# Optimization experiments

Hardware: AMD Instinct MI355X
Metric: run time of the kernel (lower is better)

## Reference

```python
import jax, jax.numpy as jnp
import numpy as np


def conv(x, w, b=None, stride=1, pad=0):
    out = jax.lax.conv_general_dilated(
        x, w, (stride, stride), ((pad, pad), (pad, pad)),
        dimension_numbers=('NCHW', 'OIHW', 'NCHW'))
    if b is not None:
        out = out + b[None, :, None, None]
    return out


def conv_transpose_4s2p1(x, w, b):
    # PyTorch ConvTranspose2d(k=4, stride=2, pad=1) == lhs-dilated conv,
    # pad = k - 1 - p = 2 each side; output spatial = 2 * input.
    out = jax.lax.conv_general_dilated(
        x, w, (1, 1), ((2, 2), (2, 2)), lhs_dilation=(2, 2),
        dimension_numbers=('NCHW', 'OIHW', 'NCHW'))
    return out + b[None, :, None, None]


def res_stack(h, blocks):
    # block: x + Conv1x1(ReLU(Conv3x3(ReLU(x)))); final ReLU after stack
    for wa, wb in blocks:
        r = conv(jax.nn.relu(h), wa, None, 1, 1)
        r = conv(jax.nn.relu(r), wb, None, 1, 0)
        h = h + r
    return jax.nn.relu(h)


def setup_inputs() -> dict:
    key = jax.random.key(0)
    ks = iter(jax.random.split(key, 32))
    H = 128  # num_hiddens
    RH = 32  # num_residual_hiddens
    K, D = 512, 64  # num_embeddings, embedding_dim
    B = 32

    def w(shape, fan_in):
        s = 1.0 / np.sqrt(fan_in)
        return jax.random.uniform(next(ks), shape, jnp.float32, -s, s)

    inp = {}
    inp['x'] = jax.random.normal(next(ks), (B, 3, 128, 128), jnp.float32)
    # encoder
    inp['e_w1'] = w((H // 2, 3, 4, 4), 3 * 16); inp['e_b1'] = w((H // 2,), 3 * 16)
    inp['e_w2'] = w((H, H // 2, 4, 4), H // 2 * 16); inp['e_b2'] = w((H,), H // 2 * 16)
    inp['e_w3'] = w((H, H, 3, 3), H * 9); inp['e_b3'] = w((H,), H * 9)
    inp['e_r1a'] = w((RH, H, 3, 3), H * 9); inp['e_r1b'] = w((H, RH, 1, 1), RH)
    inp['e_r2a'] = w((RH, H, 3, 3), H * 9); inp['e_r2b'] = w((H, RH, 1, 1), RH)
    # pre-VQ 1x1 conv
    inp['pre_w'] = w((D, H, 1, 1), H); inp['pre_b'] = w((D,), H)
    # codebook: uniform(-1/K, 1/K)
    inp['codebook'] = jax.random.uniform(next(ks), (K, D), jnp.float32, -1.0 / K, 1.0 / K)
    # decoder
    inp['d_w1'] = w((H, D, 3, 3), D * 9); inp['d_b1'] = w((H,), D * 9)
    inp['d_r1a'] = w((RH, H, 3, 3), H * 9); inp['d_r1b'] = w((H, RH, 1, 1), RH)
    inp['d_r2a'] = w((RH, H, 3, 3), H * 9); inp['d_r2b'] = w((H, RH, 1, 1), RH)
    inp['dt_w1'] = w((H // 2, H, 4, 4), H * 16); inp['dt_b1'] = w((H // 2,), H * 16)
    inp['dt_w2'] = w((3, H // 2, 4, 4), H // 2 * 16); inp['dt_b2'] = w((3,), H // 2 * 16)
    return inp


def reference(x, e_w1, e_b1, e_w2, e_b2, e_w3, e_b3, e_r1a, e_r1b, e_r2a, e_r2b,
              pre_w, pre_b, codebook, d_w1, d_b1, d_r1a, d_r1b, d_r2a, d_r2b,
              dt_w1, dt_b1, dt_w2, dt_b2):
    beta = 0.25  # commitment cost
    K = codebook.shape[0]
    # ----- encoder -----
    h = jax.nn.relu(conv(x, e_w1, e_b1, 2, 1))
    h = jax.nn.relu(conv(h, e_w2, e_b2, 2, 1))
    h = conv(h, e_w3, e_b3, 1, 1)
    h = res_stack(h, [(e_r1a, e_r1b), (e_r2a, e_r2b)])
    z = conv(h, pre_w, pre_b, 1, 0)  # [B, D, h, w]
    # ----- vector quantizer -----
    zl = jnp.transpose(z, (0, 2, 3, 1))  # [B, h, w, D]
    flat = zl.reshape(-1, zl.shape[-1])  # [N, D]
    d2 = (jnp.sum(flat * flat, axis=1, keepdims=True)
          + jnp.sum(codebook * codebook, axis=1)
          - 2.0 * flat @ codebook.T)  # [N, K]
    idx = jnp.argmin(d2, axis=1)  # [N]
    enc = jax.nn.one_hot(idx, K, dtype=flat.dtype)  # [N, K]
    q = codebook[idx].reshape(zl.shape)  # == enc @ codebook
    q_latent = jnp.mean((jax.lax.stop_gradient(q) - zl) ** 2)
    e_latent = jnp.mean((q - jax.lax.stop_gradient(zl)) ** 2)
    loss = q_latent + beta * e_latent
    q_st = zl + jax.lax.stop_gradient(q - zl)  # straight-through
    avg_probs = jnp.mean(enc, axis=0)
    perplexity = jnp.exp(-jnp.sum(avg_probs * jnp.log(avg_probs + 1e-10)))
    qc = jnp.transpose(q_st, (0, 3, 1, 2))  # [B, D, h, w]
    # ----- decoder -----
    g = conv(qc, d_w1, d_b1, 1, 1)
    g = res_stack(g, [(d_r1a, d_r1b), (d_r2a, d_r2b)])
    g = jax.nn.relu(conv_transpose_4s2p1(g, dt_w1, dt_b1))
    x_recon = conv_transpose_4s2p1(g, dt_w2, dt_b2)
    return (loss, x_recon, perplexity)
```

## Files before the change

### kernel.cpp

```cpp
#include <hip/hip_runtime.h>


typedef short short8 __attribute__((ext_vector_type(8)));
typedef float f32x4 __attribute__((ext_vector_type(4)));
typedef unsigned short us;

__device__ __forceinline__ us f2bf(float f) {
    unsigned u = __builtin_bit_cast(unsigned, f);
    u += 0x7fffu + ((u >> 16) & 1u);
    return (us)(u >> 16);
}
__device__ __forceinline__ float bf2f(us b) {
    unsigned u = ((unsigned)b) << 16;
    return __builtin_bit_cast(float, u);
}
__device__ __forceinline__ void gload_lds16(const void* g, void* l) {
    __builtin_amdgcn_global_load_lds(
        (const __attribute__((address_space(1))) void*)g,
        (__attribute__((address_space(3))) void*)l, 16, 0, 0);
}

template<bool SPLIT, int MI, int NI, int ASTR, int APLANE, int BPLANE>
__device__ __forceinline__ void mfma_step32(
    const us* lsA, const us* lsB, f32x4* acc, int wm0, int wn0, int l)
{
    short8 ah[MI], bh[NI];
    #pragma unroll
    for (int mi = 0; mi < MI; ++mi)
        ah[mi] = *(const short8*)&lsA[(wm0 + mi*16 + (l&15))*ASTR + (l>>4)*8];
    #pragma unroll
    for (int ni = 0; ni < NI; ++ni)
        bh[ni] = *(const short8*)&lsB[(wn0 + ni*16 + (l&15))*32 + (l>>4)*8];
    if (SPLIT) {
        short8 al[MI], bl[NI];
        #pragma unroll
        for (int mi = 0; mi < MI; ++mi)
            al[mi] = *(const short8*)&lsA[APLANE + (wm0 + mi*16 + (l&15))*ASTR + (l>>4)*8];
        #pragma unroll
        for (int ni = 0; ni < NI; ++ni)
            bl[ni] = *(const short8*)&lsB[BPLANE + (wn0 + ni*16 + (l&15))*32 + (l>>4)*8];
        #pragma unroll
        for (int mi = 0; mi < MI; ++mi)
            #pragma unroll
            for (int ni = 0; ni < NI; ++ni) {
                acc[mi*NI+ni] = __builtin_amdgcn_mfma_f32_16x16x32_bf16(ah[mi], bh[ni], acc[mi*NI+ni], 0, 0, 0);
                acc[mi*NI+ni] = __builtin_amdgcn_mfma_f32_16x16x32_bf16(ah[mi], bl[ni], acc[mi*NI+ni], 0, 0, 0);
                acc[mi*NI+ni] = __builtin_amdgcn_mfma_f32_16x16x32_bf16(al[mi], bh[ni], acc[mi*NI+ni], 0, 0, 0);
            }
    } else {
        #pragma unroll
        for (int mi = 0; mi < MI; ++mi)
            #pragma unroll
            for (int ni = 0; ni < NI; ++ni)
                acc[mi*NI+ni] = __builtin_amdgcn_mfma_f32_16x16x32_bf16(ah[mi], bh[ni], acc[mi*NI+ni], 0, 0, 0);
    }
}

template<int CIN, int KH, int KW, int S, bool FP32IN, bool SPLIT,
         int BN, int WM_, int WN_, bool BIAS, int RESID, bool RELU, bool DUAL,
         int OMODE, bool BK64>
__global__ __launch_bounds__(256, 4) void conv_gemm(
    const us* __restrict__ inH, const us* __restrict__ inL,
    const float* __restrict__ inF,
    const us* __restrict__ Wp, unsigned long long wloff,
    const float* __restrict__ bias,
    us* __restrict__ oH, us* __restrict__ oL,
    us* __restrict__ o2H, us* __restrict__ o2L,
    float* __restrict__ oF,
    const us* __restrict__ rH, const us* __restrict__ rL,
    const us* __restrict__ zpage,
    int Hin, int Win, int Wout, int HWout, int Cout, int pady, int padx,
    int py, int px, int nbn)
{
    constexpr int BM = 64;
    constexpr int K = CIN * KH * KW;
    constexpr int KP = ((K + 31) / 32) * 32;
    constexpr int TAPS = KH * KW;
    constexpr int ASTR = FP32IN ? 40 : 32;
    constexpr int ASHORT = FP32IN ? BM*40 : (BK64 ? BM*64 : BM*32);
    constexpr int BSHORT = (BK64 && !FP32IN) ? BN*64 : BN*32;
    constexpr int MI = BM / WM_ / 16, NI = BN / WN_ / 16;
    constexpr bool PIX1 = (KH == 1 && KW == 1 && S == 1);
    __shared__ __align__(16) us lsA[(SPLIT ? 2 : 1) * ASHORT];
    __shared__ __align__(16) us lsB[(SPLIT ? 2 : 1) * BSHORT];

    int t = threadIdx.x, l = t & 63, w = t >> 6;
    int bid = blockIdx.x;
    int nt = bid % nbn;
    int tm = (bid / nbn) * BM;
    int ncol0 = nt * BN;
    const us* Wt = Wp + (size_t)ncol0 * KP;
    int wm0 = (w / WN_) * (BM / WM_);
    int wn0 = (w % WN_) * (BN / WN_);
    f32x4 acc[MI * NI] = {};
    const int e0 = t * 8;

    if (FP32IN) {
        int m_l = t & 63, kseg = t >> 6;
        int ms = tm + m_l;
        int bsv = ms / HWout; int remv = ms - bsv * HWout;
        int oys = remv / Wout, oxs = remv - (remv / Wout) * Wout;
        int iy0 = oys * S - pady, ix0 = oxs * S - padx;
        const float* ibase = inF + (size_t)bsv * CIN * Hin * Win;
        for (int k0 = 0; k0 < KP; k0 += 32) {
            if (e0 < BN * 32) {
                size_t gb = (size_t)(e0 >> 5) * KP + k0 + (e0 & 31);
                gload_lds16(Wt + gb, &lsB[e0]);
                if (SPLIT) gload_lds16(Wt + wloff + gb, &lsB[BSHORT + e0]);
            }
            short8 hi, lo;
            #pragma unroll
            for (int j = 0; j < 8; ++j) {
                int k = k0 + kseg * 8 + j;
                float v = 0.f;
                if (k < K) {
                    int tap = k / CIN, c = k - tap * CIN;
                    int ky = tap / KW, kx = tap - (tap / KW) * KW;
                    int iy = iy0 + ky, ix = ix0 + kx;
                    if ((unsigned)iy < (unsigned)Hin && (unsigned)ix < (unsigned)Win)
                        v = ibase[((size_t)c * Hin + iy) * Win + ix];
                }
                us hb = f2bf(v);
                hi[j] = (short)hb;
                if (SPLIT) lo[j] = (short)f2bf(v - bf2f(hb));
            }
            *(short8*)&lsA[m_l * ASTR + kseg * 8] = hi;
            if (SPLIT) *(short8*)&lsA[ASHORT + m_l * ASTR + kseg * 8] = lo;
            __syncthreads();
            mfma_step32<SPLIT, MI, NI, ASTR, ASHORT, BSHORT>(lsA, lsB, acc, wm0, wn0, l);
            __syncthreads();
        }
    } else if (!BK64) {
        int mrow = t >> 2;
        int lane8 = (t & 3) * 8;
        int m = tm + mrow;
        int bsv = m / HWout; int remv = m - bsv * HWout;
        int oys = remv / Wout, oxs = remv - oys * Wout;
        int iy0 = oys * S - pady, ix0 = oxs * S - padx;
        #pragma unroll
        for (int tap = 0; tap < TAPS; ++tap) {
            int ky = tap / KW, kx = tap - (tap / KW) * KW;
            int iy = iy0 + ky, ix = ix0 + kx;
            bool ok = PIX1 || ((unsigned)iy < (unsigned)Hin && (unsigned)ix < (unsigned)Win);
            size_t pix = ((size_t)bsv * Hin + iy) * Win + ix;
            const us* phi = ok ? inH + pix * CIN + lane8 : zpage + lane8;
            const us* plo = zpage;
            if (SPLIT) plo = ok ? inL + pix * CIN + lane8 : zpage + lane8;
            #pragma unroll
            for (int cc = 0; cc < CIN; cc += 32) {
                const int k0 = tap * CIN + cc;
                if (e0 < BN * 32) {
                    size_t gb = (size_t)(e0 >> 5) * KP + k0 + (e0 & 31);
                    gload_lds16(Wt + gb, &lsB[e0]);
                    if (SPLIT) gload_lds16(Wt + wloff + gb, &lsB[BSHORT + e0]);
                }
                gload_lds16(phi + cc, &lsA[t * 8]);
                if (SPLIT) gload_lds16(plo + cc, &lsA[ASHORT + t * 8]);
                __syncthreads();
                mfma_step32<SPLIT, MI, NI, ASTR, ASHORT, BSHORT>(lsA, lsB, acc, wm0, wn0, l);
                __syncthreads();
            }
        }
    } else {
        int r0 = t >> 3;
        int lc8 = (((t & 7) ^ (t >> 3)) & 7) * 8;
        int m0v = tm + r0, m1v = tm + r0 + 32;
        int bs0 = m0v / HWout, rm0 = m0v - bs0 * HWout;
        int oy0 = rm0 / Wout, ox0 = rm0 - oy0 * Wout;
        int bs1 = m1v / HWout, rm1 = m1v - bs1 * HWout;
        int oy1 = rm1 / Wout, ox1 = rm1 - oy1 * Wout;
        int iy00 = oy0 * S - pady, ix00 = ox0 * S - padx;
        int iy10 = oy1 * S - pady, ix10 = ox1 * S - padx;
        #pragma unroll
        for (int tap = 0; tap < TAPS; ++tap) {
            int ky = tap / KW, kx = tap - (tap / KW) * KW;
            int iyA = iy00 + ky, ixA = ix00 + kx;
            int iyB = iy10 + ky, ixB = ix10 + kx;
            bool okA = PIX1 || ((unsigned)iyA < (unsigned)Hin && (unsigned)ixA < (unsigned)Win);
            bool okB = PIX1 || ((unsigned)iyB < (unsigned)Hin && (unsigned)ixB < (unsigned)Win);
            size_t pxA = ((size_t)bs0 * Hin + iyA) * Win + ixA;
            size_t pxB = ((size_t)bs1 * Hin + iyB) * Win + ixB;
            const us* pA = okA ? inH + pxA * CIN + lc8 : zpage + lc8;
            const us* pB = okB ? inH + pxB * CIN + lc8 : zpage + lc8;
            const us* qA = zpage + lc8;
            const us* qB = zpage + lc8;
            if (SPLIT) {
                qA = okA ? inL + pxA * CIN + lc8 : zpage + lc8;
                qB = okB ? inL + pxB * CIN + lc8 : zpage + lc8;
            }
            #pragma unroll
            for (int cc = 0; cc < CIN; cc += 64) {
                const int k0 = tap * CIN + cc;
                #pragma unroll
                for (int q = 0; q < (BN + 31) / 32; ++q) {
                    if (BN >= 32 || t < BN * 8) {
                        size_t gb = (size_t)(q * 32 + (t >> 3)) * KP + k0 + (t & 7) * 8;
                        gload_lds16(Wt + gb, &lsB[q * 2048 + t * 8]);
                        if (SPLIT) gload_lds16(Wt + wloff + gb, &lsB[BSHORT + q * 2048 + t * 8]);
                    }
                }
                gload_lds16(pA + cc, &lsA[t * 8]);
                gload_lds16(pB + cc, &lsA[2048 + t * 8]);
                if (SPLIT) {
                    gload_lds16(qA + cc, &lsA[ASHORT + t * 8]);
                    gload_lds16(qB + cc, &lsA[ASHORT + 2048 + t * 8]);
                }
                __syncthreads();
                #pragma unroll
                for (int kk = 0; kk < 2; ++kk) {
                    short8 ah[MI], bh[NI];
                    #pragma unroll
                    for (int mi = 0; mi < MI; ++mi) {
                        int row = wm0 + mi * 16 + (l & 15);
                        int pc = (kk * 4 + (l >> 4)) ^ (row & 7);
                        ah[mi] = *(const short8*)&lsA[row * 64 + pc * 8];
                    }
                    #pragma unroll
                    for (int ni = 0; ni < NI; ++ni) {
                        int row = wn0 + ni * 16 + (l & 15);
                        int pc = (kk * 4 + (l >> 4)) ^ (row & 7);
                        bh[ni] = *(const short8*)&lsB[row * 64 + pc * 8];
                    }
                    if (SPLIT) {
                        short8 al[MI], bl[NI];
                        #pragma unroll
                        for (int mi = 0; mi < MI; ++mi) {
                            int row = wm0 + mi * 16 + (l & 15);
                            int pc = (kk * 4 + (l >> 4)) ^ (row & 7);
                            al[mi] = *(const short8*)&lsA[ASHORT + row * 64 + pc * 8];
                        }
                        #pragma unroll
                        for (int ni = 0; ni < NI; ++ni) {
                            int row = wn0 + ni * 16 + (l & 15);
                            int pc = (kk * 4 + (l >> 4)) ^ (row & 7);
                            bl[ni] = *(const short8*)&lsB[BSHORT + row * 64 + pc * 8];
                        }
                        #pragma unroll
                        for (int mi = 0; mi < MI; ++mi)
                            #pragma unroll
                            for (int ni = 0; ni < NI; ++ni) {
                                acc[mi*NI+ni] = __builtin_amdgcn_mfma_f32_16x16x32_bf16(ah[mi], bh[ni], acc[mi*NI+ni], 0, 0, 0);
                                acc[mi*NI+ni] = __builtin_amdgcn_mfma_f32_16x16x32_bf16(ah[mi], bl[ni], acc[mi*NI+ni], 0, 0, 0);
                                acc[mi*NI+ni] = __builtin_amdgcn_mfma_f32_16x16x32_bf16(al[mi], bh[ni], acc[mi*NI+ni], 0, 0, 0);
                            }
                    } else {
                        #pragma unroll
                        for (int mi = 0; mi < MI; ++mi)
                            #pragma unroll
                            for (int ni = 0; ni < NI; ++ni)
                                acc[mi*NI+ni] = __builtin_amdgcn_mfma_f32_16x16x32_bf16(ah[mi], bh[ni], acc[mi*NI+ni], 0, 0, 0);
                    }
                }
                __syncthreads();
            }
        }
    }

    #pragma unroll
    for (int mi = 0; mi < MI; ++mi) {
        #pragma unroll
        for (int ni = 0; ni < NI; ++ni) {
            int n = ncol0 + wn0 + ni * 16 + (l & 15);
            if (n >= Cout) continue;
            float bv = BIAS ? bias[n] : 0.f;
            #pragma unroll
            for (int j = 0; j < 4; ++j) {
                int m = tm + wm0 + mi * 16 + (l >> 4) * 4 + j;
                float v = acc[mi * NI + ni][j] + bv;
                if (RESID == 1) { size_t ri = (size_t)m * Cout + n; v += bf2f(rH[ri]) + bf2f(rL[ri]); }
                if (RESID == 2) { v += bf2f(rH[(size_t)m * Cout + n]); }
                float vr = RELU ? fmaxf(v, 0.f) : v;
                if (DUAL) {
                    size_t oi = (size_t)m * Cout + n;
                    us hb = f2bf(v);
                    o2H[oi] = hb;
                    if (SPLIT) o2L[oi] = f2bf(v - bf2f(hb));
                }
                if (OMODE == 0) {
                    size_t oi = (size_t)m * Cout + n;
                    us hb = f2bf(vr);
                    oH[oi] = hb;
                    if (SPLIT) oL[oi] = f2bf(vr - bf2f(hb));
                } else if (OMODE == 1) {
                    int b2 = m / HWout, rem = m - b2 * HWout;
                    oF[(size_t)(b2 * Cout + n) * HWout + rem] = vr;
                } else if (OMODE == 2) {
                    int b2 = m / HWout, rem = m - b2 * HWout;
                    int y = rem / Wout, x2 = rem - y * Wout;
                    oF[(size_t)(b2 * Cout + n) * (4 * HWout)
                       + (size_t)(2 * y + py) * (2 * Wout) + (2 * x2 + px)] = vr;
                } else {
                    int b2 = m / HWout, rem = m - b2 * HWout;
                    int y = rem / Wout, x2 = rem - y * Wout;
                    int Hg2 = 2 * (HWout / Wout);
                    size_t oi = (((size_t)b2 * Hg2 + (2 * y + py)) * (size_t)(2 * Wout)
                                 + (2 * x2 + px)) * Cout + n;
                    oH[oi] = f2bf(vr);
                }
            }
        }
    }
}

struct PackDesc {
    const float* src; unsigned long long dstoff;
    int Npad, N, CIN, KH, KW, K, Kpad, mode, py, px, split, swz;
};
struct PackArgs { PackDesc d[21]; };

__global__ __launch_bounds__(256) void wpack_all(PackArgs pa, us* __restrict__ wp)
{
    PackDesc d = pa.d[blockIdx.y];
    int gid = blockIdx.x * 256 + threadIdx.x;
    int tot = d.Npad * d.Kpad;
    if (gid >= tot) return;
    int n = gid / d.Kpad;
    int k = gid - n * d.Kpad;
    int klog = k;
    if (d.swz) {
        int kb = k >> 6, pc = (k >> 3) & 7, j = k & 7;
        klog = (kb << 6) + (((pc ^ (n & 7)) & 7) << 3) + j;
    }
    float v = 0.0f;
    if (n < d.N && klog < d.K) {
        int tap = klog / d.CIN, c = klog - tap * d.CIN;
        int ky, kx;
        if (d.mode == 0) { ky = tap / d.KW; kx = tap - (tap / d.KW) * d.KW; }
        else { int ty = tap >> 1, tx = tap & 1; ky = d.py + 2 * ty; kx = d.px + 2 * tx; }
        v = d.src[((size_t)(n * d.CIN + c) * d.KH + ky) * d.KW + kx];
    }
    us hb = f2bf(v);
    wp[d.dstoff + gid] = hb;
    if (d.split) wp[d.dstoff + tot + gid] = f2bf(v - bf2f(hb));
}

__global__ __launch_bounds__(256) void vq_sq(
    const float* __restrict__ cb, float* __restrict__ ccsq)
{
    int k = blockIdx.x * 256 + threadIdx.x;
    const float* c = cb + (size_t)k * 64;
    float a0 = 0.f, a1 = 0.f;
    #pragma unroll
    for (int d = 0; d < 64; d += 2) {
        a0 = fmaf(c[d], c[d], a0);
        a1 = fmaf(c[d + 1], c[d + 1], a1);
    }
    ccsq[k] = a0 + a1;
}

__global__ __launch_bounds__(256) void vq_scan(
    const float* __restrict__ z, const float* __restrict__ cb,
    const float* __restrict__ ccsq,
    float* __restrict__ pdist, int* __restrict__ pidx)
{
    const int HW = 1024;
    int n = blockIdx.x * 256 + threadIdx.x;
    int chunk = blockIdx.y;
    int base = chunk * 64;
    int b = n >> 10;
    int p = n & 1023;
    const float* zp = z + (size_t)b * 64 * HW + p;
    float zv[64];
    #pragma unroll
    for (int d = 0; d < 64; ++d) zv[d] = zp[(size_t)d * HW];

    float best = 3.402823e38f;
    int bi = base;
    for (int kk = 0; kk < 64; kk += 2) {
        const float* c0 = cb + (size_t)(base + kk) * 64;
        float a0 = 0.f, a1 = 0.f, b0 = 0.f, b1 = 0.f;
        #pragma unroll
        for (int d = 0; d < 64; d += 2) {
            a0 = fmaf(zv[d],     c0[d],          a0);
            a1 = fmaf(zv[d + 1], c0[d + 1],      a1);
            b0 = fmaf(zv[d],     c0[64 + d],     b0);
            b1 = fmaf(zv[d + 1], c0[64 + d + 1], b1);
        }
        float s0 = ccsq[base + kk]     - 2.0f * (a0 + a1);
        float s1 = ccsq[base + kk + 1] - 2.0f * (b0 + b1);
        if (s0 < best) { best = s0; bi = base + kk; }
        if (s1 < best) { best = s1; bi = base + kk + 1; }
    }
    pdist[(size_t)chunk * 32768 + n] = best;
    pidx [(size_t)chunk * 32768 + n] = bi;
}

__global__ __launch_bounds__(256) void vq_reduce(
    const float* __restrict__ z, const float* __restrict__ cb,
    const float* __restrict__ pdist, const int* __restrict__ pidx,
    us* __restrict__ qb, int* __restrict__ idxbuf, float* __restrict__ sse)
{
    const int HW = 1024;
    int nl = threadIdx.x & 31;
    int dg = threadIdx.x >> 5;
    int n = blockIdx.x * 32 + nl;
    float best = pdist[n];
    int bi = pidx[n];
    #pragma unroll
    for (int ch = 1; ch < 8; ++ch) {
        float dv = pdist[(size_t)ch * 32768 + n];
        int iv = pidx[(size_t)ch * 32768 + n];
        if (dv < best) { best = dv; bi = iv; }
    }
    if (dg == 0) idxbuf[n] = bi;
    int b = n >> 10;
    int p = n & 1023;
    const float* zp = z + (size_t)b * 64 * HW + p;
    const float* c = cb + (size_t)bi * 64;
    float s = 0.f;
    short8 qv;
    #pragma unroll
    for (int j = 0; j < 8; ++j) {
        int d = dg * 8 + j;
        float q = c[d];
        qv[j] = (short)f2bf(q);
        float df = q - zp[(size_t)d * HW];
        s = fmaf(df, df, s);
    }
    *(short8*)&qb[(size_t)n * 64 + dg * 8] = qv;
    #pragma unroll
    for (int off = 32; off > 0; off >>= 1) s += __shfl_down(s, off, 64);
    __shared__ float red[4];
    if ((threadIdx.x & 63) == 0) red[threadIdx.x >> 6] = s;
    __syncthreads();
    if (threadIdx.x == 0) atomicAdd(sse, red[0] + red[1] + red[2] + red[3]);
}

__global__ __launch_bounds__(1024) void vq_hist(
    const int* __restrict__ idxbuf, float* __restrict__ hist)
{
    __shared__ int lh[512];
    int t = threadIdx.x;
    if (t < 512) lh[t] = 0;
    __syncthreads();
    #pragma unroll
    for (int j = 0; j < 32; ++j)
        atomicAdd(&lh[idxbuf[j * 1024 + t]], 1);
    __syncthreads();
    if (t < 512) hist[t] = (float)lh[t];
}

__global__ __launch_bounds__(512) void vq_finalize(
    const float* __restrict__ hist, const float* __restrict__ sse,
    float* __restrict__ out_loss, float* __restrict__ out_ppl)
{
    __shared__ float red[512];
    int t = threadIdx.x;
    float p = hist[t] * (1.0f / 32768.0f);
    red[t] = p * logf(p + 1e-10f);
    __syncthreads();
    for (int s = 256; s > 0; s >>= 1) {
        if (t < s) red[t] += red[t + s];
        __syncthreads();
    }
    if (t == 0) {
        *out_ppl = expf(-red[0]);
        *out_loss = 1.25f * (*sse) * (1.0f / 2097152.0f);
    }
}

extern "C" void kernel_launch(void* const* d_in, const int* in_sizes, int n_in,
                              void* d_out, int out_size, void* d_ws, size_t ws_size,
                              hipStream_t stream)
{
    const float* x        = (const float*)d_in[0];
    const float* e_w1     = (const float*)d_in[1];
    const float* e_b1     = (const float*)d_in[2];
    const float* e_w2     = (const float*)d_in[3];
    const float* e_b2     = (const float*)d_in[4];
    const float* e_w3     = (const float*)d_in[5];
    const float* e_b3     = (const float*)d_in[6];
    const float* e_r1a    = (const float*)d_in[7];
    const float* e_r1b    = (const float*)d_in[8];
    const float* e_r2a    = (const float*)d_in[9];
    const float* e_r2b    = (const float*)d_in[10];
    const float* pre_w    = (const float*)d_in[11];
    const float* pre_b    = (const float*)d_in[12];
    const float* codebook = (const float*)d_in[13];
    const float* d_w1     = (const float*)d_in[14];
    const float* d_b1     = (const float*)d_in[15];
    const float* d_r1a    = (const float*)d_in[16];
    const float* d_r1b    = (const float*)d_in[17];
    const float* d_r2a    = (const float*)d_in[18];
    const float* d_r2b    = (const float*)d_in[19];
    const float* dt_w1    = (const float*)d_in[20];
    const float* dt_b1    = (const float*)d_in[21];
    const float* dt_w2    = (const float*)d_in[22];
    const float* dt_b2    = (const float*)d_in[23];
    float* out = (float*)d_out;

    const size_t MB = 1024 * 1024;
    char* base = (char*)d_ws;
    char* A0 = base;
    char* B0 = base + 32 * MB;
    char* C0 = base + 48 * MB;
    char* D0 = base + 64 * MB;
    float* st = (float*)(base + 68 * MB);
    us* wp = (us*)(base + 68 * MB + 4096);

    us* h1H = (us*)A0;              us* h1L = (us*)(A0 + 16 * MB);
    us* hBH = (us*)B0;              us* hBL = (us*)(B0 + 8 * MB);
    us* CeH = (us*)A0;              us* CeL = (us*)(A0 + 8 * MB);
    us* CrH = (us*)C0;              us* CrL = (us*)(C0 + 8 * MB);
    us* DsH = (us*)D0;              us* DsL = (us*)(D0 + 2 * MB);
    us* T2rH = (us*)A0;             us* T2rL = (us*)(A0 + 8 * MB);
    us* T2eH = (us*)B0;             us* T2eL = (us*)(B0 + 8 * MB);
    us* T3H = (us*)C0;              us* T3L = (us*)(C0 + 8 * MB);
    float* E = (float*)B0;
    us* qb = (us*)(B0 + 8 * MB);
    float* pdist = (float*)A0;
    int* pidx = (int*)(A0 + 1 * MB);
    int* idxbuf = (int*)(A0 + 2 * MB);
    float* ccsq = (float*)(A0 + 2 * MB + 128 * 1024);
    us* GeH = (us*)A0;              us* GrH = (us*)(A0 + 8 * MB);
    us* dDs = (us*)D0;
    us* dT2e = (us*)B0;             us* dT2r = (us*)(B0 + 8 * MB);
    us* dT3 = (us*)C0;
    us* gbuf = (us*)A0;
    const us* zpage = (const us*)(st + 576);

    PackArgs pa;
    int np = 0; unsigned long long wpo = 0;
    auto addpack = [&](const float* src, int N, int Npad, int CIN, int KH, int KW,
                       int K, int Kpad, int mode, int py, int px, int split,
                       int swz) -> unsigned long long {
        pa.d[np].src = src; pa.d[np].dstoff = wpo;
        pa.d[np].Npad = Npad; pa.d[np].N = N; pa.d[np].CIN = CIN;
        pa.d[np].KH = KH; pa.d[np].KW = KW; pa.d[np].K = K; pa.d[np].Kpad = Kpad;
        pa.d[np].mode = mode; pa.d[np].py = py; pa.d[np].px = px;
        pa.d[np].split = split; pa.d[np].swz = swz;
        ++np; unsigned long long off = wpo; wpo += (unsigned long long)Npad * Kpad * (split ? 2 : 1);
        return off;
    };
    unsigned long long P_E1  = addpack(e_w1, 64, 64, 3, 4, 4, 48, 64, 0, 0, 0, 1, 0);
    unsigned long long P_E2  = addpack(e_w2, 128, 128, 64, 4, 4, 1024, 1024, 0, 0, 0, 1, 1);
    unsigned long long P_E3  = addpack(e_w3, 128, 128, 128, 3, 3, 1152, 1152, 0, 0, 0, 1, 1);
    unsigned long long P_R1A = addpack(e_r1a, 32, 32, 128, 3, 3, 1152, 1152, 0, 0, 0, 1, 1);
    unsigned long long P_R1B = addpack(e_r1b, 128, 128, 32, 1, 1, 32, 32, 0, 0, 0, 1, 0);
    unsigned long long P_R2A = addpack(e_r2a, 32, 32, 128, 3, 3, 1152, 1152, 0, 0, 0, 1, 1);
    unsigned long long P_R2B = addpack(e_r2b, 128, 128, 32, 1, 1, 32, 32, 0, 0, 0, 1, 0);
    unsigned long long P_PRE = addpack(pre_w, 64, 64, 128, 1, 1, 128, 128, 0, 0, 0, 1, 1);
    unsigned long long P_D1  = addpack(d_w1, 128, 128, 64, 3, 3, 576, 576, 0, 0, 0, 0, 1);
    unsigned long long P_DR1A = addpack(d_r1a, 32, 32, 128, 3, 3, 1152, 1152, 0, 0, 0, 0, 1);
    unsigned long long P_DR1B = addpack(d_r1b, 128, 128, 32, 1, 1, 32, 32, 0, 0, 0, 0, 0);
    unsigned long long P_DR2A = addpack(d_r2a, 32, 32, 128, 3, 3, 1152, 1152, 0, 0, 0, 0, 1);
    unsigned long long P_DR2B = addpack(d_r2b, 128, 128, 32, 1, 1, 32, 32, 0, 0, 0, 0, 0);
    unsigned long long P_DT1[4], P_DT2[4];
    for (int p = 0; p < 4; ++p)
        P_DT1[p] = addpack(dt_w1, 64, 64, 128, 4, 4, 512, 512, 1, p >> 1, p & 1, 0, 1);
    for (int p = 0; p < 4; ++p)
        P_DT2[p] = addpack(dt_w2, 3, 16, 64, 4, 4, 256, 256, 1, p >> 1, p & 1, 0, 1);

    hipMemsetAsync(st, 0, 4096, stream);
    wpack_all<<<dim3(576, 21), 256, 0, stream>>>(pa, wp);

    conv_gemm<3,4,4,2, true,true, 64,2,2, true,0,true,false,0, false><<<dim3(2048),256,0,stream>>>(
        nullptr, nullptr, x, wp + P_E1, 64ull*64, e_b1,
        h1H, h1L, nullptr, nullptr, nullptr, nullptr, nullptr, zpage,
        128,128, 64, 4096, 64, 1,1, 0,0, 1);
    conv_gemm<64,4,4,2, false,true, 64,2,2, true,0,true,false,0, true><<<dim3(1024),256,0,stream>>>(
        h1H, h1L, nullptr, wp + P_E2, 128ull*1024, e_b2,
        hBH, hBL, nullptr, nullptr, nullptr, nullptr, nullptr, zpage,
        64,64, 32, 1024, 128, 1,1, 0,0, 2);
    conv_gemm<128,3,3,1, false,true, 64,2,2, true,0,true,true,0, true><<<dim3(1024),256,0,stream>>>(
        hBH, hBL, nullptr, wp + P_E3, 128ull*1152, e_b3,
        CeH, CeL, CrH, CrL, nullptr, nullptr, nullptr, zpage,
        32,32, 32, 1024, 128, 1,1, 0,0, 2);
    conv_gemm<128,3,3,1, false,true, 32,4,1, false,0,true,false,0, true><<<dim3(512),256,0,stream>>>(
        CeH, CeL, nullptr, wp + P_R1A, 32ull*1152, nullptr,
        DsH, DsL, nullptr, nullptr, nullptr, nullptr, nullptr, zpage,
        32,32, 32, 1024, 32, 1,1, 0,0, 1);
    conv_gemm<32,1,1,1, false,true, 64,2,2, false,1,true,true,0, false><<<dim3(1024),256,0,stream>>>(
        DsH, DsL, nullptr, wp + P_R1B, 128ull*32, nullptr,
        T2eH, T2eL, T2rH, T2rL, nullptr, CrH, CrL, zpage,
        32,32, 32, 1024, 128, 0,0, 0,0, 2);
    conv_gemm<128,3,3,1, false,true, 32,4,1, false,0,true,false,0, true><<<dim3(512),256,0,stream>>>(
        T2eH, T2eL, nullptr, wp + P_R2A, 32ull*1152, nullptr,
        DsH, DsL, nullptr, nullptr, nullptr, nullptr, nullptr, zpage,
        32,32, 32, 1024, 32, 1,1, 0,0, 1);
    conv_gemm<32,1,1,1, false,true, 64,2,2, false,1,true,false,0, false><<<dim3(1024),256,0,stream>>>(
        DsH, DsL, nullptr, wp + P_R2B, 128ull*32, nullptr,
        T3H, T3L, nullptr, nullptr, nullptr, T2rH, T2rL, zpage,
        32,32, 32, 1024, 128, 0,0, 0,0, 2);
    conv_gemm<128,1,1,1, false,true, 64,2,2, true,0,false,false,1, true><<<dim3(512),256,0,stream>>>(
        T3H, T3L, nullptr, wp + P_PRE, 64ull*128, pre_b,
        nullptr, nullptr, nullptr, nullptr, E, nullptr, nullptr, zpage,
        32,32, 32, 1024, 64, 0,0, 0,0, 1);

    vq_sq<<<dim3(2), 256, 0, stream>>>(codebook, ccsq);
    vq_scan<<<dim3(128, 8), 256, 0, stream>>>(E, codebook, ccsq, pdist, pidx);
    vq_reduce<<<dim3(1024), 256, 0, stream>>>(E, codebook, pdist, pidx, qb, idxbuf, st + 512);
    vq_hist<<<dim3(1), 1024, 0, stream>>>(idxbuf, st);
    vq_finalize<<<dim3(1), 512, 0, stream>>>(st, st + 512, out, out + 1572865);

    conv_gemm<64,3,3,1, false,false, 64,2,2, true,0,true,true,0, true><<<dim3(1024),256,0,stream>>>(
        qb, nullptr, nullptr, wp + P_D1, 0ull, d_b1,
        GeH, nullptr, GrH, nullptr, nullptr, nullptr, nullptr, zpage,
        32,32, 32, 1024, 128, 1,1, 0,0, 2);
    conv_gemm<128,3,3,1, false,false, 32,4,1, false,0,true,false,0, true><<<dim3(512),256,0,stream>>>(
        GeH, nullptr, nullptr, wp + P_DR1A, 0ull, nullptr,
        dDs, nullptr, nullptr, nullptr, nullptr, nullptr, nullptr, zpage,
        32,32, 32, 1024, 32, 1,1, 0,0, 1);
    conv_gemm<32,1,1,1, false,false, 64,2,2, false,2,true,true,0, false><<<dim3(1024),256,0,stream>>>(
        dDs, nullptr, nullptr, wp + P_DR1B, 0ull, nullptr,
        dT2e, nullptr, dT2r, nullptr, nullptr, GrH, nullptr, zpage,
        32,32, 32, 1024, 128, 0,0, 0,0, 2);
    conv_gemm<128,3,3,1, false,false, 32,4,1, false,0,true,false,0, true><<<dim3(512),256,0,stream>>>(
        dT2e, nullptr, nullptr, wp + P_DR2A, 0ull, nullptr,
        dDs, nullptr, nullptr, nullptr, nullptr, nullptr, nullptr, zpage,
        32,32, 32, 1024, 32, 1,1, 0,0, 1);
    conv_gemm<32,1,1,1, false,false, 64,2,2, false,2,true,false,0, false><<<dim3(1024),256,0,stream>>>(
        dDs, nullptr, nullptr, wp + P_DR2B, 0ull, nullptr,
        dT3, nullptr, nullptr, nullptr, nullptr, dT2r, nullptr, zpage,
        32,32, 32, 1024, 128, 0,0, 0,0, 2);
    for (int p = 0; p < 4; ++p) {
        conv_gemm<128,2,2,1, false,false, 64,2,2, true,0,true,false,3, true><<<dim3(512),256,0,stream>>>(
            dT3, nullptr, nullptr, wp + P_DT1[p], 0ull, dt_b1,
            gbuf, nullptr, nullptr, nullptr, nullptr, nullptr, nullptr, zpage,
            32,32, 32, 1024, 64, 1-(p>>1), 1-(p&1), p>>1, p&1, 1);
    }
    for (int p = 0; p < 4; ++p) {
        conv_gemm<64,2,2,1, false,false, 16,4,1, true,0,false,false,2, true><<<dim3(2048),256,0,stream>>>(
            gbuf, nullptr, nullptr, wp + P_DT2[p], 0ull, dt_b2,
            nullptr, nullptr, nullptr, nullptr, out + 1, nullptr, nullptr, zpage,
            64,64, 64, 4096, 3, 1-(p>>1), 1-(p&1), p>>1, p&1, 1);
    }
}
```

Baseline: 456.0 us.

## Batch transposed-conv parities into one launch, merge VQ tail, widen BN tiles

The four parity launches of each transposed conv become one 2D-grid launch, with blockIdx.y picking the parity, its pad and offset values, and its packed weight slice. The VQ histogram and finalize kernels become a single kernel, dropping one launch and the global round-trip of the histogram. Several encoder and decoder 3x3/4x4 convs move from BN=64 with two N-tiles to BN=128 with one N-tile, halving their grid size. The weight offset par*BN*KP assumes the per-parity packs are laid out contiguously with exactly that stride, which the addpack layout must match.

```diff
diff --git a/kernel.cpp b/kernel.cpp
--- a/kernel.cpp
+++ b/kernel.cpp
@@ -58,7 +58,7 @@
 
 template<int CIN, int KH, int KW, int S, bool FP32IN, bool SPLIT,
          int BN, int WM_, int WN_, bool BIAS, int RESID, bool RELU, bool DUAL,
-         int OMODE, bool BK64>
+         int OMODE, bool BK64, bool PMULTI>
 __global__ __launch_bounds__(256, 4) void conv_gemm(
     const us* __restrict__ inH, const us* __restrict__ inL,
     const float* __restrict__ inF,
@@ -89,7 +89,13 @@
     int nt = bid % nbn;
     int tm = (bid / nbn) * BM;
     int ncol0 = nt * BN;
-    const us* Wt = Wp + (size_t)ncol0 * KP;
+    int par = 0;
+    if (PMULTI) {
+        par = blockIdx.y;
+        pady = 1 - (par >> 1); padx = 1 - (par & 1);
+        py = par >> 1;         px = par & 1;
+    }
+    const us* Wt = Wp + (size_t)par * BN * KP + (size_t)ncol0 * KP;
     int wm0 = (w / WN_) * (BM / WM_);
     int wn0 = (w % WN_) * (BN / WN_);
     f32x4 acc[MI * NI] = {};
@@ -426,10 +432,12 @@
     if (threadIdx.x == 0) atomicAdd(sse, red[0] + red[1] + red[2] + red[3]);
 }
 
-__global__ __launch_bounds__(1024) void vq_hist(
-    const int* __restrict__ idxbuf, float* __restrict__ hist)
+__global__ __launch_bounds__(1024) void vq_hist_fin(
+    const int* __restrict__ idxbuf, const float* __restrict__ sse,
+    float* __restrict__ out_loss, float* __restrict__ out_ppl)
 {
     __shared__ int lh[512];
+    __shared__ float red[512];
     int t = threadIdx.x;
     if (t < 512) lh[t] = 0;
     __syncthreads();
@@ -437,17 +445,10 @@
     for (int j = 0; j < 32; ++j)
         atomicAdd(&lh[idxbuf[j * 1024 + t]], 1);
     __syncthreads();
-    if (t < 512) hist[t] = (float)lh[t];
-}
-
-__global__ __launch_bounds__(512) void vq_finalize(
-    const float* __restrict__ hist, const float* __restrict__ sse,
-    float* __restrict__ out_loss, float* __restrict__ out_ppl)
-{
-    __shared__ float red[512];
-    int t = threadIdx.x;
-    float p = hist[t] * (1.0f / 32768.0f);
-    red[t] = p * logf(p + 1e-10f);
+    if (t < 512) {
+        float p = (float)lh[t] * (1.0f / 32768.0f);
+        red[t] = p * logf(p + 1e-10f);
+    }
     __syncthreads();
     for (int s = 256; s > 0; s >>= 1) {
         if (t < s) red[t] += red[t + s];
@@ -554,35 +555,35 @@
     hipMemsetAsync(st, 0, 4096, stream);
     wpack_all<<<dim3(576, 21), 256, 0, stream>>>(pa, wp);
 
-    conv_gemm<3,4,4,2, true,true, 64,2,2, true,0,true,false,0, false><<<dim3(2048),256,0,stream>>>(
+    conv_gemm<3,4,4,2, true,true, 64,2,2, true,0,true,false,0, false,false><<<dim3(2048),256,0,stream>>>(
         nullptr, nullptr, x, wp + P_E1, 64ull*64, e_b1,
         h1H, h1L, nullptr, nullptr, nullptr, nullptr, nullptr, zpage,
         128,128, 64, 4096, 64, 1,1, 0,0, 1);
-    conv_gemm<64,4,4,2, false,true, 64,2,2, true,0,true,false,0, true><<<dim3(1024),256,0,stream>>>(
+    conv_gemm<64,4,4,2, false,true, 128,2,2, true,0,true,false,0, true,false><<<dim3(512),256,0,stream>>>(
         h1H, h1L, nullptr, wp + P_E2, 128ull*1024, e_b2,
         hBH, hBL, nullptr, nullptr, nullptr, nullptr, nullptr, zpage,
-        64,64, 32, 1024, 128, 1,1, 0,0, 2);
-    conv_gemm<128,3,3,1, false,true, 64,2,2, true,0,true,true,0, true><<<dim3(1024),256,0,stream>>>(
+        64,64, 32, 1024, 128, 1,1, 0,0, 1);
+    conv_gemm<128,3,3,1, false,true, 128,2,2, true,0,true,true,0, true,false><<<dim3(512),256,0,stream>>>(
         hBH, hBL, nullptr, wp + P_E3, 128ull*1152, e_b3,
         CeH, CeL, CrH, CrL, nullptr, nullptr, nullptr, zpage,
-        32,32, 32, 1024, 128, 1,1, 0,0, 2);
-    conv_gemm<128,3,3,1, false,true, 32,4,1, false,0,true,false,0, true><<<dim3(512),256,0,stream>>>(
+        32,32, 32, 1024, 128, 1,1, 0,0, 1);
+    conv_gemm<128,3,3,1, false,true, 32,4,1, false,0,true,false,0, true,false><<<dim3(512),256,0,stream>>>(
         CeH, CeL, nullptr, wp + P_R1A, 32ull*1152, nullptr,
         DsH, DsL, nullptr, nullptr, nullptr, nullptr, nullptr, zpage,
         32,32, 32, 1024, 32, 1,1, 0,0, 1);
-    conv_gemm<32,1,1,1, false,true, 64,2,2, false,1,true,true,0, false><<<dim3(1024),256,0,stream>>>(
+    conv_gemm<32,1,1,1, false,true, 64,2,2, false,1,true,true,0, false,false><<<dim3(1024),256,0,stream>>>(
         DsH, DsL, nullptr, wp + P_R1B, 128ull*32, nullptr,
         T2eH, T2eL, T2rH, T2rL, nullptr, CrH, CrL, zpage,
         32,32, 32, 1024, 128, 0,0, 0,0, 2);
-    conv_gemm<128,3,3,1, false,true, 32,4,1, false,0,true,false,0, true><<<dim3(512),256,0,stream>>>(
+    conv_gemm<128,3,3,1, false,true, 32,4,1, false,0,true,false,0, true,false><<<dim3(512),256,0,stream>>>(
         T2eH, T2eL, nullptr, wp + P_R2A, 32ull*1152, nullptr,
         DsH, DsL, nullptr, nullptr, nullptr, nullptr, nullptr, zpage,
         32,32, 32, 1024, 32, 1,1, 0,0, 1);
-    conv_gemm<32,1,1,1, false,true, 64,2,2, false,1,true,false,0, false><<<dim3(1024),256,0,stream>>>(
+    conv_gemm<32,1,1,1, false,true, 64,2,2, false,1,true,false,0, false,false><<<dim3(1024),256,0,stream>>>(
         DsH, DsL, nullptr, wp + P_R2B, 128ull*32, nullptr,
         T3H, T3L, nullptr, nullptr, nullptr, T2rH, T2rL, zpage,
         32,32, 32, 1024, 128, 0,0, 0,0, 2);
-    conv_gemm<128,1,1,1, false,true, 64,2,2, true,0,false,false,1, true><<<dim3(512),256,0,stream>>>(
+    conv_gemm<128,1,1,1, false,true, 64,2,2, true,0,false,false,1, true,false><<<dim3(512),256,0,stream>>>(
         T3H, T3L, nullptr, wp + P_PRE, 64ull*128, pre_b,
         nullptr, nullptr, nullptr, nullptr, E, nullptr, nullptr, zpage,
         32,32, 32, 1024, 64, 0,0, 0,0, 1);
@@ -590,39 +591,34 @@
     vq_sq<<<dim3(2), 256, 0, stream>>>(codebook, ccsq);
     vq_scan<<<dim3(128, 8), 256, 0, stream>>>(E, codebook, ccsq, pdist, pidx);
     vq_reduce<<<dim3(1024), 256, 0, stream>>>(E, codebook, pdist, pidx, qb, idxbuf, st + 512);
-    vq_hist<<<dim3(1), 1024, 0, stream>>>(idxbuf, st);
-    vq_finalize<<<dim3(1), 512, 0, stream>>>(st, st + 512, out, out + 1572865);
-
-    conv_gemm<64,3,3,1, false,false, 64,2,2, true,0,true,true,0, true><<<dim3(1024),256,0,stream>>>(
+    vq_hist_fin<<<dim3(1), 1024, 0, stream>>>(idxbuf, st + 512, out, out + 1572865);
+
+    conv_gemm<64,3,3,1, false,false, 128,2,2, true,0,true,true,0, true,false><<<dim3(512),256,0,stream>>>(
         qb, nullptr, nullptr, wp + P_D1, 0ull, d_b1,
         GeH, nullptr, GrH, nullptr, nullptr, nullptr, nullptr, zpage,
-        32,32, 32, 1024, 128, 1,1, 0,0, 2);
-    conv_gemm<128,3,3,1, false,false, 32,4,1, false,0,true,false,0, true><<<dim3(512),256,0,stream>>>(
+        32,32, 32, 1024, 128, 1,1, 0,0, 1);
+    conv_gemm<128,3,3,1, false,false, 32,4,1, false,0,true,false,0, true,false><<<dim3(512),256,0,stream>>>(
         GeH, nullptr, nullptr, wp + P_DR1A, 0ull, nullptr,
         dDs, nullptr, nullptr, nullptr, nullptr, nullptr, nullptr, zpage,
         32,32, 32, 1024, 32, 1,1, 0,0, 1);
-    conv_gemm<32,1,1,1, false,false, 64,2,2, false,2,true,true,0, false><<<dim3(1024),256,0,stream>>>(
+    conv_gemm<32,1,1,1, false,false, 64,2,2, false,2,true,true,0, false,false><<<dim3(1024),256,0,stream>>>(
         dDs, nullptr, nullptr, wp + P_DR1B, 0ull, nullptr,
         dT2e, nullptr, dT2r, nullptr, nullptr, GrH, nullptr, zpage,
         32,32, 32, 1024, 128, 0,0, 0,0, 2);
-    conv_gemm<128,3,3,1, false,false, 32,4,1, false,0,true,false,0, true><<<dim3(512),256,0,stream>>>(
+    conv_gemm<128,3,3,1, false,false, 32,4,1, false,0,true,false,0, true,false><<<dim3(512),256,0,stream>>>(
         dT2e, nullptr, nullptr, wp + P_DR2A, 0ull, nullptr,
         dDs, nullptr, nullptr, nullptr, nullptr, nullptr, nullptr, zpage,
         32,32, 32, 1024, 32, 1,1, 0,0, 1);
-    conv_gemm<32,1,1,1, false,false, 64,2,2, false,2,true,false,0, false><<<dim3(1024),256,0,stream>>>(
+    conv_gemm<32,1,1,1, false,false, 64,2,2, false,2,true,false,0, false,false><<<dim3(1024),256,0,stream>>>(
         dDs, nullptr, nullptr, wp + P_DR2B, 0ull, nullptr,
         dT3, nullptr, nullptr, nullptr, nullptr, dT2r, nullptr, zpage,
         32,32, 32, 1024, 128, 0,0, 0,0, 2);
-    for (int p = 0; p < 4; ++p) {
-        conv_gemm<128,2,2,1, false,false, 64,2,2, true,0,true,false,3, true><<<dim3(512),256,0,stream>>>(
-            dT3, nullptr, nullptr, wp + P_DT1[p], 0ull, dt_b1,
-            gbuf, nullptr, nullptr, nullptr, nullptr, nullptr, nullptr, zpage,
-            32,32, 32, 1024, 64, 1-(p>>1), 1-(p&1), p>>1, p&1, 1);
-    }
-    for (int p = 0; p < 4; ++p) {
-        conv_gemm<64,2,2,1, false,false, 16,4,1, true,0,false,false,2, true><<<dim3(2048),256,0,stream>>>(
-            gbuf, nullptr, nullptr, wp + P_DT2[p], 0ull, dt_b2,
-            nullptr, nullptr, nullptr, nullptr, out + 1, nullptr, nullptr, zpage,
-            64,64, 64, 4096, 3, 1-(p>>1), 1-(p&1), p>>1, p&1, 1);
-    }
-}
+    conv_gemm<128,2,2,1, false,false, 64,2,2, true,0,true,false,3, true,true><<<dim3(512,4),256,0,stream>>>(
+        dT3, nullptr, nullptr, wp + P_DT1[0], 0ull, dt_b1,
+        gbuf, nullptr, nullptr, nullptr, nullptr, nullptr, nullptr, zpage,
+        32,32, 32, 1024, 64, 0,0, 0,0, 1);
+    conv_gemm<64,2,2,1, false,false, 16,4,1, true,0,false,false,2, true,true><<<dim3(2048,4),256,0,stream>>>(
+        gbuf, nullptr, nullptr, wp + P_DT2[0], 0ull, dt_b2,
+        nullptr, nullptr, nullptr, nullptr, out + 1, nullptr, nullptr, zpage,
+        64,64, 64, 4096, 3, 0,0, 0,0, 1);
+}
```

New measurement: 422.9 us. 7.3% less time.
